# Optimization experiments

Measured on AMD Instinct MI355X. Metric: run time of the kernel, lower is better.

The kernel has to match this reference:

```python
import jax, jax.numpy as jnp
import numpy as np

B, S, D = 2, 2048, 1024
H, HD = 16, 64  # num_heads, hidden_size per head


def setup_inputs() -> dict:
    key = jax.random.key(0)
    ks = jax.random.split(key, 10)
    inp = {
        'queries': jax.random.normal(ks[0], (B, S, D), jnp.float32),
        'keys': jax.random.normal(ks[1], (B, S, D), jnp.float32),
        'values': jax.random.normal(ks[2], (B, S, D), jnp.float32),
        # binary indicator masks (some zeros so renorm guard path is exercised)
        'ind_q': (jax.random.uniform(ks[3], (B, S)) > 0.2).astype(jnp.float32),
        'ind_k': (jax.random.uniform(ks[4], (B, S)) > 0.2).astype(jnp.float32),
        'ind_v': (jax.random.uniform(ks[5], (B, S)) > 0.2).astype(jnp.float32),
        'Wq': jax.random.normal(ks[6], (D, H * HD), jnp.float32) / np.sqrt(D),
        'Wk': jax.random.normal(ks[7], (D, H * HD), jnp.float32) / np.sqrt(D),
        'Wv': jax.random.normal(ks[8], (D, H * HD), jnp.float32) / np.sqrt(D),
        'Wo': jax.random.normal(ks[9], (H * HD, D), jnp.float32) / np.sqrt(H * HD),
    }
    return inp


def reference(queries, keys, values, ind_q, ind_k, ind_v, Wq, Wk, Wv, Wo):
    b, nq, _ = queries.shape
    nk = keys.shape[1]
    # projections -> [B, H, S, HD], masked by indicators
    Q = (queries @ Wq).reshape(b, nq, H, HD).transpose(0, 2, 1, 3) * ind_q[:, None, :, None]
    K = (keys @ Wk).reshape(b, nk, H, HD).transpose(0, 2, 1, 3) * ind_k[:, None, :, None]
    V = (values @ Wv).reshape(b, nk, H, HD).transpose(0, 2, 1, 3) * ind_v[:, None, :, None]
    # scaled dot-product scores, plain softmax over keys
    scores = jnp.einsum('bhqd,bhkd->bhqk', Q, K) / jnp.sqrt(jnp.float32(HD))
    attn = jax.nn.softmax(scores, axis=-1)
    # post-softmax multiplicative key-indicator mask + renormalization with zero-row guard
    attn = attn * ind_k[:, None, None, :]
    denom = jnp.sum(attn, axis=-1, keepdims=True)
    attn = attn / jnp.where(denom == 0.0, 1.0, denom)
    out = jnp.einsum('bhqk,bhkd->bhqd', attn, V)  # [B, H, Q, HD]
    out = out.transpose(0, 2, 1, 3).reshape(b, nq, H * HD)
    return out @ Wo
```

## Files before the change

### kernel.cpp

```cpp
#include <hip/hip_runtime.h>
#include <math.h>

typedef __attribute__((ext_vector_type(8))) short bf16x8;
typedef __attribute__((ext_vector_type(4))) float f32x4;

__device__ __forceinline__ unsigned short f2b(float f) {
    union { float f; unsigned int u; } v; v.f = f;
    unsigned int u = v.u + 0x7FFFu + ((v.u >> 16) & 1u);
    return (unsigned short)(u >> 16);
}

__device__ __forceinline__ unsigned int pack2bf(float a, float b) {
    union { float f; unsigned int u; } ua, ub; ua.f = a; ub.f = b;
    return __builtin_amdgcn_perm(ub.u + 0x8000u, ua.u + 0x8000u, 0x07060302u);
}

__device__ __forceinline__ f32x4 mfma16(bf16x8 a, bf16x8 b, f32x4 c) {
    return __builtin_amdgcn_mfma_f32_16x16x32_bf16(a, b, c, 0, 0, 0);
}

__device__ __forceinline__ void async_ld16(void* l, const void* g) {
    __builtin_amdgcn_global_load_lds(
        (__attribute__((address_space(1))) void*)g,
        (__attribute__((address_space(3))) void*)l, 16, 0, 0);
}

__global__ __launch_bounds__(256) void cvt3(
    const float* __restrict__ q, const float* __restrict__ k,
    const float* __restrict__ v, unsigned short* __restrict__ qo,
    unsigned short* __restrict__ ko, unsigned short* __restrict__ vo)
{
    const int z = blockIdx.z;
    const float* in = (z == 0) ? q : (z == 1) ? k : v;
    unsigned short* out = (z == 0) ? qo : (z == 1) ? ko : vo;
    const int i = (blockIdx.x * 256 + threadIdx.x) * 4;
    const float4 x = *(const float4*)(in + i);
    ushort4 o; o.x = f2b(x.x); o.y = f2b(x.y); o.z = f2b(x.z); o.w = f2b(x.w);
    *(ushort4*)(out + i) = o;
}

__global__ __launch_bounds__(256) void cvt_tr(
    const float* __restrict__ W0, const float* __restrict__ W1,
    const float* __restrict__ W2, const float* __restrict__ W3,
    unsigned short* __restrict__ T0, unsigned short* __restrict__ T1,
    unsigned short* __restrict__ T2, unsigned short* __restrict__ T3)
{
    const int z = blockIdx.z;
    const float* W = (z == 0) ? W0 : (z == 1) ? W1 : (z == 2) ? W2 : W3;
    unsigned short* T = (z == 0) ? T0 : (z == 1) ? T1 : (z == 2) ? T2 : T3;
    __shared__ short Ls[64 * 65];
    const int t = threadIdx.x;
    const int k0 = blockIdx.x * 64, n0 = blockIdx.y * 64;
#pragma unroll
    for (int ii = 0; ii < 4; ++ii) {
        const int kl = (t >> 4) + 16 * ii, nl = (t & 15) * 4;
        const float4 v = *(const float4*)&W[(size_t)(k0 + kl) * 1024 + n0 + nl];
        Ls[kl * 65 + nl + 0] = (short)f2b(v.x);
        Ls[kl * 65 + nl + 1] = (short)f2b(v.y);
        Ls[kl * 65 + nl + 2] = (short)f2b(v.z);
        Ls[kl * 65 + nl + 3] = (short)f2b(v.w);
    }
    __syncthreads();
#pragma unroll
    for (int ii = 0; ii < 4; ++ii) {
        const int nl = (t >> 4) + 16 * ii, kl = (t & 15) * 4;
        ushort4 o;
        o.x = (unsigned short)Ls[(kl + 0) * 65 + nl];
        o.y = (unsigned short)Ls[(kl + 1) * 65 + nl];
        o.z = (unsigned short)Ls[(kl + 2) * 65 + nl];
        o.w = (unsigned short)Ls[(kl + 3) * 65 + nl];
        *(ushort4*)&T[(size_t)(n0 + nl) * 1024 + k0 + kl] = o;
    }
}

__global__ __launch_bounds__(256) void gemm_proj3(
    const unsigned short* __restrict__ qb, const unsigned short* __restrict__ kb,
    const unsigned short* __restrict__ vb,
    const unsigned short* __restrict__ Wqt, const unsigned short* __restrict__ Wkt,
    const unsigned short* __restrict__ Wvt,
    unsigned short* __restrict__ Qw, unsigned short* __restrict__ Kw,
    unsigned short* __restrict__ Vw,
    const float* __restrict__ iq, const float* __restrict__ ik,
    const float* __restrict__ iv)
{
    const int z = blockIdx.z;
    const unsigned short* A  = (z == 0) ? qb  : (z == 1) ? kb  : vb;
    const unsigned short* Bt = (z == 0) ? Wqt : (z == 1) ? Wkt : Wvt;
    unsigned short* Cw       = (z == 0) ? Qw  : (z == 1) ? Kw  : Vw;
    const float* msk         = (z == 0) ? iq  : (z == 1) ? ik  : iv;
    const float scale = (z == 0) ? 0.125f : 1.0f;

    __shared__ __align__(16) short As[128 * 32];
    __shared__ __align__(16) short Bs[128 * 32];
    __shared__ float maskL[128];
    const int t = threadIdx.x;
    const int w = t >> 6, lane = t & 63, l15 = lane & 15, quad = lane >> 4;
    const int wr = w >> 1, wc = w & 1;
    const int n0 = blockIdx.x * 128, m0 = blockIdx.y * 128;
    if (t < 128) maskL[t] = msk[m0 + t] * scale;

    const int srow = lane >> 2, soff = (lane & 3) * 8;

    f32x4 zero4 = {0.f, 0.f, 0.f, 0.f};
    f32x4 acc[4][4];
#pragma unroll
    for (int i = 0; i < 4; ++i)
#pragma unroll
        for (int j = 0; j < 4; ++j) acc[i][j] = zero4;

    for (int k0 = 0; k0 < 1024; k0 += 32) {
        __syncthreads();
#pragma unroll
        for (int i = 0; i < 2; ++i) {
            const int r = 16 * (2 * w + i);
            async_ld16(As + r * 32, A + (size_t)(m0 + r + srow) * 1024 + k0 + soff);
            async_ld16(Bs + r * 32, Bt + (size_t)(n0 + r + srow) * 1024 + k0 + soff);
        }
        __syncthreads();
        bf16x8 af[4], bfr[4];
#pragma unroll
        for (int i = 0; i < 4; ++i)
            af[i] = *(const bf16x8*)&As[(64 * wr + 16 * i + l15) * 32 + 8 * quad];
#pragma unroll
        for (int j = 0; j < 4; ++j)
            bfr[j] = *(const bf16x8*)&Bs[(64 * wc + 16 * j + l15) * 32 + 8 * quad];
#pragma unroll
        for (int i = 0; i < 4; ++i)
#pragma unroll
            for (int j = 0; j < 4; ++j)
                acc[i][j] = mfma16(af[i], bfr[j], acc[i][j]);
    }

    const int h = 2 * blockIdx.x + wc;
#pragma unroll
    for (int i = 0; i < 4; ++i)
#pragma unroll
        for (int j = 0; j < 4; ++j)
#pragma unroll
            for (int reg = 0; reg < 4; ++reg) {
                const int mloc = 64 * wr + 16 * i + 4 * quad + reg;
                const int m = m0 + mloc;
                const int bb = m >> 11, s = m & 2047;
                const int hd = 16 * j + l15;
                Cw[((size_t)(bb * 16 + h) * 2048 + s) * 64 + hd] =
                    f2b(acc[i][j][reg] * maskL[mloc]);
            }
}

__global__ __launch_bounds__(256) void gemm_out(
    const unsigned short* __restrict__ A, const unsigned short* __restrict__ Bt,
    float* __restrict__ C)
{
    __shared__ __align__(16) short As[128 * 32];
    __shared__ __align__(16) short Bs[64 * 32];
    const int t = threadIdx.x;
    const int w = t >> 6, lane = t & 63, l15 = lane & 15, quad = lane >> 4;
    const int wr = w >> 1, wc = w & 1;
    const int n0 = blockIdx.x * 64, m0 = blockIdx.y * 128;
    const int srow = lane >> 2, soff = (lane & 3) * 8;

    f32x4 zero4 = {0.f, 0.f, 0.f, 0.f};
    f32x4 acc[4][2];
#pragma unroll
    for (int i = 0; i < 4; ++i) { acc[i][0] = zero4; acc[i][1] = zero4; }

    for (int k0 = 0; k0 < 1024; k0 += 32) {
        __syncthreads();
#pragma unroll
        for (int i = 0; i < 2; ++i) {
            const int r = 16 * (2 * w + i);
            async_ld16(As + r * 32, A + (size_t)(m0 + r + srow) * 1024 + k0 + soff);
        }
        async_ld16(Bs + (16 * w) * 32, Bt + (size_t)(n0 + 16 * w + srow) * 1024 + k0 + soff);
        __syncthreads();
        bf16x8 af[4], bfr[2];
#pragma unroll
        for (int i = 0; i < 4; ++i)
            af[i] = *(const bf16x8*)&As[(64 * wr + 16 * i + l15) * 32 + 8 * quad];
#pragma unroll
        for (int j = 0; j < 2; ++j)
            bfr[j] = *(const bf16x8*)&Bs[(32 * wc + 16 * j + l15) * 32 + 8 * quad];
#pragma unroll
        for (int i = 0; i < 4; ++i)
#pragma unroll
            for (int j = 0; j < 2; ++j)
                acc[i][j] = mfma16(af[i], bfr[j], acc[i][j]);
    }
#pragma unroll
    for (int i = 0; i < 4; ++i)
#pragma unroll
        for (int j = 0; j < 2; ++j)
#pragma unroll
            for (int reg = 0; reg < 4; ++reg) {
                const int m = m0 + 64 * wr + 16 * i + 4 * quad + reg;
                const int n = n0 + 32 * wc + 16 * j + l15;
                C[(size_t)m * 1024 + n] = acc[i][j][reg];
            }
}

#define GST 72

__global__ __launch_bounds__(512, 4) void attn_mfma(
    const unsigned short* __restrict__ Qw, const unsigned short* __restrict__ Kw,
    const unsigned short* __restrict__ Vw, const float* __restrict__ indk,
    unsigned short* __restrict__ AO)
{
    __shared__ __align__(16) short Ks[2][64 * GST];
    __shared__ __align__(16) short Vt[2][64 * GST];
    __shared__ __align__(16) short Ps[128 * GST];
    __shared__ float biask[2][64];
    const int t = threadIdx.x;
    const int w = t >> 6, lane = t & 63, l15 = lane & 15, quad = lane >> 4;
    const int q0 = blockIdx.x * 128;
    const int h = blockIdx.y, b = blockIdx.z;
    const size_t base = (size_t)(b * 16 + h) * (2048 * 64);
    const unsigned short* Qb = Qw + base + (size_t)q0 * 64;
    const unsigned short* Kb = Kw + base;
    const unsigned short* Vb = Vw + base;

#pragma unroll
    for (int i = 0; i < 4; ++i) {
        const int idx = t + 512 * i;
        const int r = idx >> 4, dg = (idx & 15) * 4;
        *(ushort4*)&Ps[r * GST + dg] = *(const ushort4*)&Qb[r * 64 + dg];
    }
    ushort4 kreg[2], vreg[2];
    float breg = 0.f;
#pragma unroll
    for (int u = 0; u < 2; ++u) {
        const int idx = t + 512 * u;
        kreg[u] = *(const ushort4*)&Kb[(size_t)(idx >> 4) * 64 + (idx & 15) * 4];
        vreg[u] = *(const ushort4*)&Vb[(size_t)(idx & 63) * 64 + (idx >> 6) * 4];
    }
    if (t < 64) breg = indk[b * 2048 + t];
    __syncthreads();
    bf16x8 qf[2];
    qf[0] = *(const bf16x8*)&Ps[(16 * w + l15) * GST + 8 * quad];
    qf[1] = *(const bf16x8*)&Ps[(16 * w + l15) * GST + 32 + 8 * quad];

    f32x4 zero4 = {0.f, 0.f, 0.f, 0.f};
    f32x4 oacc[4];
    oacc[0] = zero4; oacc[1] = zero4; oacc[2] = zero4; oacc[3] = zero4;
    float m_i = -INFINITY, l_i = 0.f;

    for (int c = 0; c < 32; ++c) {
        const int cur = c & 1;
#pragma unroll
        for (int u = 0; u < 2; ++u) {
            const int idx = t + 512 * u;
            const int r = idx >> 4, dg = (idx & 15) * 4;
            *(ushort4*)&Ks[cur][r * GST + dg] = kreg[u];
            const int key = idx & 63, dq = idx >> 6;
            Vt[cur][(4 * dq + 0) * GST + key] = vreg[u].x;
            Vt[cur][(4 * dq + 1) * GST + key] = vreg[u].y;
            Vt[cur][(4 * dq + 2) * GST + key] = vreg[u].z;
            Vt[cur][(4 * dq + 3) * GST + key] = vreg[u].w;
        }
        if (t < 64) biask[cur][t] = (breg != 0.f) ? 0.f : -1e30f;
        __syncthreads();
        {
            const int kn = (c < 31 ? c + 1 : 31) * 64;
#pragma unroll
            for (int u = 0; u < 2; ++u) {
                const int idx = t + 512 * u;
                kreg[u] = *(const ushort4*)&Kb[(size_t)(kn + (idx >> 4)) * 64 + (idx & 15) * 4];
                vreg[u] = *(const ushort4*)&Vb[(size_t)(kn + (idx & 63)) * 64 + (idx >> 6) * 4];
            }
            if (t < 64) breg = indk[b * 2048 + kn + t];
        }
        const short* KsC = Ks[cur];
        const short* VtC = Vt[cur];

        f32x4 sacc[4];
        sacc[0] = zero4; sacc[1] = zero4; sacc[2] = zero4; sacc[3] = zero4;
#pragma unroll
        for (int ks = 0; ks < 2; ++ks)
#pragma unroll
            for (int nj = 0; nj < 4; ++nj) {
                const bf16x8 kf = *(const bf16x8*)&KsC[(16 * nj + l15) * GST + 32 * ks + 8 * quad];
                sacc[nj] = mfma16(kf, qf[ks], sacc[nj]);
            }

#pragma unroll
        for (int nj = 0; nj < 4; ++nj) {
            const float4 bv = *(const float4*)&biask[cur][16 * nj + 4 * quad];
            sacc[nj][0] += bv.x; sacc[nj][1] += bv.y;
            sacc[nj][2] += bv.z; sacc[nj][3] += bv.w;
        }

        float mx = -INFINITY;
#pragma unroll
        for (int nj = 0; nj < 4; ++nj)
#pragma unroll
            for (int r = 0; r < 4; ++r) mx = fmaxf(mx, sacc[nj][r]);
        mx = fmaxf(mx, __shfl_xor(mx, 16));
        mx = fmaxf(mx, __shfl_xor(mx, 32));
        const float mnew = fmaxf(fmaxf(m_i, mx), -1e28f);
        const float alpha = __expf(m_i - mnew);
        float rs = 0.f;
#pragma unroll
        for (int nj = 0; nj < 4; ++nj)
#pragma unroll
            for (int r = 0; r < 4; ++r) {
                const float p = __expf(sacc[nj][r] - mnew);
                sacc[nj][r] = p;
                rs += p;
            }
        rs += __shfl_xor(rs, 16);
        rs += __shfl_xor(rs, 32);
        l_i = l_i * alpha + rs;
        m_i = mnew;

#pragma unroll
        for (int nj = 0; nj < 4; ++nj) {
            uint2 d;
            d.x = pack2bf(sacc[nj][0], sacc[nj][1]);
            d.y = pack2bf(sacc[nj][2], sacc[nj][3]);
            *(uint2*)&Ps[(16 * w + l15) * GST + 16 * nj + 4 * quad] = d;
        }

        float ar[4];
#pragma unroll
        for (int r = 0; r < 4; ++r) ar[r] = __shfl(alpha, 4 * quad + r);
#pragma unroll
        for (int nj = 0; nj < 4; ++nj)
#pragma unroll
            for (int r = 0; r < 4; ++r) oacc[nj][r] *= ar[r];

#pragma unroll
        for (int ks = 0; ks < 2; ++ks) {
            const bf16x8 pa = *(const bf16x8*)&Ps[(16 * w + l15) * GST + 32 * ks + 8 * quad];
#pragma unroll
            for (int nj = 0; nj < 4; ++nj) {
                const bf16x8 vbf = *(const bf16x8*)&VtC[(16 * nj + l15) * GST + 32 * ks + 8 * quad];
                oacc[nj] = mfma16(pa, vbf, oacc[nj]);
            }
        }
    }

    const float inv = (l_i > 0.f) ? 1.f / l_i : 0.f;
    float invr[4];
#pragma unroll
    for (int r = 0; r < 4; ++r) invr[r] = __shfl(inv, 4 * quad + r);
#pragma unroll
    for (int nj = 0; nj < 4; ++nj)
#pragma unroll
        for (int r = 0; r < 4; ++r) {
            const int row = q0 + 16 * w + 4 * quad + r;
            AO[(size_t)(b * 2048 + row) * 1024 + h * 64 + 16 * nj + l15] =
                f2b(oacc[nj][r] * invr[r]);
        }
}

extern "C" void kernel_launch(void* const* d_in, const int* in_sizes, int n_in,
                              void* d_out, int out_size, void* d_ws, size_t ws_size,
                              hipStream_t stream) {
    const float* q  = (const float*)d_in[0];
    const float* k  = (const float*)d_in[1];
    const float* v  = (const float*)d_in[2];
    const float* iq = (const float*)d_in[3];
    const float* ik = (const float*)d_in[4];
    const float* iv = (const float*)d_in[5];
    const float* Wq = (const float*)d_in[6];
    const float* Wk = (const float*)d_in[7];
    const float* Wv = (const float*)d_in[8];
    const float* Wo = (const float*)d_in[9];
    float* out = (float*)d_out;
    unsigned short* ws = (unsigned short*)d_ws;

    const size_t M1 = 1048576;
    unsigned short* qb  = ws;
    unsigned short* kb  = ws + 4  * M1;
    unsigned short* vb  = ws + 8  * M1;
    unsigned short* Wqt = ws + 12 * M1;
    unsigned short* Wkt = ws + 13 * M1;
    unsigned short* Wvt = ws + 14 * M1;
    unsigned short* Wot = ws + 15 * M1;
    unsigned short* Qw  = ws + 16 * M1;
    unsigned short* Kw  = ws + 20 * M1;
    unsigned short* Vw  = ws + 24 * M1;
    unsigned short* AO  = ws + 28 * M1;

    cvt3<<<dim3(4096, 1, 3), dim3(256), 0, stream>>>(q, k, v, qb, kb, vb);
    cvt_tr<<<dim3(16, 16, 4), dim3(256), 0, stream>>>(Wq, Wk, Wv, Wo, Wqt, Wkt, Wvt, Wot);
    gemm_proj3<<<dim3(8, 32, 3), dim3(256), 0, stream>>>(
        qb, kb, vb, Wqt, Wkt, Wvt, Qw, Kw, Vw, iq, ik, iv);
    attn_mfma<<<dim3(16, 16, 2), dim3(512), 0, stream>>>(Qw, Kw, Vw, ik, AO);
    gemm_out<<<dim3(16, 32), dim3(256), 0, stream>>>(AO, Wot, out);
}
```

Before: 256.1 us.

## Keep P in registers, fold log2e into Q, lazy rescale, packed V transpose

Removes the shared-memory round trip for the softmax probabilities. The S accumulator rows are permuted so that each lane's P values can feed the PV MFMA directly as operands. The log2(e) factor is folded into the Q projection scale, so exponentials use the hardware v_exp_f32 and packing uses v_cvt_pk_bf16_f32. The online-softmax rescale of the output accumulator is skipped unless the running max grows by more than 8. The V transpose now writes packed dword stores built with byte permutes, and Q is loaded straight from global into registers. s_setprio hints are placed around the MFMA blocks. This cuts LDS traffic and ALU work, at the cost of bounded growth in the unnormalised exponentials.

```diff
diff --git a/kernel.cpp b/kernel.cpp
--- a/kernel.cpp
+++ b/kernel.cpp
@@ -10,11 +10,6 @@
     return (unsigned short)(u >> 16);
 }
 
-__device__ __forceinline__ unsigned int pack2bf(float a, float b) {
-    union { float f; unsigned int u; } ua, ub; ua.f = a; ub.f = b;
-    return __builtin_amdgcn_perm(ub.u + 0x8000u, ua.u + 0x8000u, 0x07060302u);
-}
-
 __device__ __forceinline__ f32x4 mfma16(bf16x8 a, bf16x8 b, f32x4 c) {
     return __builtin_amdgcn_mfma_f32_16x16x32_bf16(a, b, c, 0, 0, 0);
 }
@@ -23,6 +18,16 @@
     __builtin_amdgcn_global_load_lds(
         (__attribute__((address_space(1))) void*)g,
         (__attribute__((address_space(3))) void*)l, 16, 0, 0);
+}
+
+__device__ __forceinline__ float exp2_hw(float x) {
+    float r; asm("v_exp_f32 %0, %1" : "=v"(r) : "v"(x)); return r;
+}
+
+__device__ __forceinline__ unsigned int cvtpk_bf16(float a, float b) {
+    unsigned int r;
+    asm("v_cvt_pk_bf16_f32 %0, %1, %2" : "=v"(r) : "v"(a), "v"(b));
+    return r;
 }
 
 __global__ __launch_bounds__(256) void cvt3(
@@ -88,7 +93,7 @@
     const unsigned short* Bt = (z == 0) ? Wqt : (z == 1) ? Wkt : Wvt;
     unsigned short* Cw       = (z == 0) ? Qw  : (z == 1) ? Kw  : Vw;
     const float* msk         = (z == 0) ? iq  : (z == 1) ? ik  : iv;
-    const float scale = (z == 0) ? 0.125f : 1.0f;
+    const float scale = (z == 0) ? 0.125f * 1.44269504088896f : 1.0f;
 
     __shared__ __align__(16) short As[128 * 32];
     __shared__ __align__(16) short Bs[128 * 32];
@@ -207,7 +212,6 @@
 {
     __shared__ __align__(16) short Ks[2][64 * GST];
     __shared__ __align__(16) short Vt[2][64 * GST];
-    __shared__ __align__(16) short Ps[128 * GST];
     __shared__ float biask[2][64];
     const int t = threadIdx.x;
     const int w = t >> 6, lane = t & 63, l15 = lane & 15, quad = lane >> 4;
@@ -218,25 +222,24 @@
     const unsigned short* Kb = Kw + base;
     const unsigned short* Vb = Vw + base;
 
-#pragma unroll
-    for (int i = 0; i < 4; ++i) {
-        const int idx = t + 512 * i;
-        const int r = idx >> 4, dg = (idx & 15) * 4;
-        *(ushort4*)&Ps[r * GST + dg] = *(const ushort4*)&Qb[r * 64 + dg];
-    }
+    bf16x8 qf[2];
+    qf[0] = *(const bf16x8*)&Qb[(16 * w + l15) * 64 + 8 * quad];
+    qf[1] = *(const bf16x8*)&Qb[(16 * w + l15) * 64 + 32 + 8 * quad];
+
+    const int dq = t >> 5, kp2 = (t & 31) * 2;
+
     ushort4 kreg[2], vreg[2];
     float breg = 0.f;
 #pragma unroll
     for (int u = 0; u < 2; ++u) {
         const int idx = t + 512 * u;
         kreg[u] = *(const ushort4*)&Kb[(size_t)(idx >> 4) * 64 + (idx & 15) * 4];
-        vreg[u] = *(const ushort4*)&Vb[(size_t)(idx & 63) * 64 + (idx >> 6) * 4];
-    }
+    }
+    vreg[0] = *(const ushort4*)&Vb[(size_t)kp2 * 64 + 4 * dq];
+    vreg[1] = *(const ushort4*)&Vb[(size_t)(kp2 + 1) * 64 + 4 * dq];
     if (t < 64) breg = indk[b * 2048 + t];
-    __syncthreads();
-    bf16x8 qf[2];
-    qf[0] = *(const bf16x8*)&Ps[(16 * w + l15) * GST + 8 * quad];
-    qf[1] = *(const bf16x8*)&Ps[(16 * w + l15) * GST + 32 + 8 * quad];
+
+    const int rbase = 8 * (l15 >> 2) + (l15 & 3);
 
     f32x4 zero4 = {0.f, 0.f, 0.f, 0.f};
     f32x4 oacc[4];
@@ -248,13 +251,19 @@
 #pragma unroll
         for (int u = 0; u < 2; ++u) {
             const int idx = t + 512 * u;
-            const int r = idx >> 4, dg = (idx & 15) * 4;
-            *(ushort4*)&Ks[cur][r * GST + dg] = kreg[u];
-            const int key = idx & 63, dq = idx >> 6;
-            Vt[cur][(4 * dq + 0) * GST + key] = vreg[u].x;
-            Vt[cur][(4 * dq + 1) * GST + key] = vreg[u].y;
-            Vt[cur][(4 * dq + 2) * GST + key] = vreg[u].z;
-            Vt[cur][(4 * dq + 3) * GST + key] = vreg[u].w;
+            *(ushort4*)&Ks[cur][(idx >> 4) * GST + (idx & 15) * 4] = kreg[u];
+        }
+        {
+            const unsigned int* v0d = (const unsigned int*)&vreg[0];
+            const unsigned int* v1d = (const unsigned int*)&vreg[1];
+            *(unsigned int*)&Vt[cur][(4 * dq + 0) * GST + kp2] =
+                __builtin_amdgcn_perm(v1d[0], v0d[0], 0x05040100u);
+            *(unsigned int*)&Vt[cur][(4 * dq + 1) * GST + kp2] =
+                __builtin_amdgcn_perm(v1d[0], v0d[0], 0x07060302u);
+            *(unsigned int*)&Vt[cur][(4 * dq + 2) * GST + kp2] =
+                __builtin_amdgcn_perm(v1d[1], v0d[1], 0x05040100u);
+            *(unsigned int*)&Vt[cur][(4 * dq + 3) * GST + kp2] =
+                __builtin_amdgcn_perm(v1d[1], v0d[1], 0x07060302u);
         }
         if (t < 64) biask[cur][t] = (breg != 0.f) ? 0.f : -1e30f;
         __syncthreads();
@@ -264,78 +273,87 @@
             for (int u = 0; u < 2; ++u) {
                 const int idx = t + 512 * u;
                 kreg[u] = *(const ushort4*)&Kb[(size_t)(kn + (idx >> 4)) * 64 + (idx & 15) * 4];
-                vreg[u] = *(const ushort4*)&Vb[(size_t)(kn + (idx & 63)) * 64 + (idx >> 6) * 4];
             }
+            vreg[0] = *(const ushort4*)&Vb[(size_t)(kn + kp2) * 64 + 4 * dq];
+            vreg[1] = *(const ushort4*)&Vb[(size_t)(kn + kp2 + 1) * 64 + 4 * dq];
             if (t < 64) breg = indk[b * 2048 + kn + t];
         }
         const short* KsC = Ks[cur];
         const short* VtC = Vt[cur];
 
         f32x4 sacc[4];
-        sacc[0] = zero4; sacc[1] = zero4; sacc[2] = zero4; sacc[3] = zero4;
+#pragma unroll
+        for (int g = 0; g < 4; ++g) {
+            const float4 bv = *(const float4*)&biask[cur][32 * (g >> 1) + 4 * (g & 1) + 8 * quad];
+            sacc[g][0] = bv.x; sacc[g][1] = bv.y; sacc[g][2] = bv.z; sacc[g][3] = bv.w;
+        }
+        __builtin_amdgcn_s_setprio(1);
 #pragma unroll
         for (int ks = 0; ks < 2; ++ks)
 #pragma unroll
-            for (int nj = 0; nj < 4; ++nj) {
-                const bf16x8 kf = *(const bf16x8*)&KsC[(16 * nj + l15) * GST + 32 * ks + 8 * quad];
-                sacc[nj] = mfma16(kf, qf[ks], sacc[nj]);
+            for (int g = 0; g < 4; ++g) {
+                const bf16x8 kf = *(const bf16x8*)
+                    &KsC[(32 * (g >> 1) + 4 * (g & 1) + rbase) * GST + 32 * ks + 8 * quad];
+                sacc[g] = mfma16(kf, qf[ks], sacc[g]);
             }
-
-#pragma unroll
-        for (int nj = 0; nj < 4; ++nj) {
-            const float4 bv = *(const float4*)&biask[cur][16 * nj + 4 * quad];
-            sacc[nj][0] += bv.x; sacc[nj][1] += bv.y;
-            sacc[nj][2] += bv.z; sacc[nj][3] += bv.w;
-        }
-
-        float mx = -INFINITY;
-#pragma unroll
-        for (int nj = 0; nj < 4; ++nj)
-#pragma unroll
-            for (int r = 0; r < 4; ++r) mx = fmaxf(mx, sacc[nj][r]);
+        __builtin_amdgcn_s_setprio(0);
+
+        float mg[4];
+#pragma unroll
+        for (int g = 0; g < 4; ++g)
+            mg[g] = fmaxf(fmaxf(sacc[g][0], sacc[g][1]), fmaxf(sacc[g][2], sacc[g][3]));
+        float mx = fmaxf(fmaxf(mg[0], mg[1]), fmaxf(mg[2], mg[3]));
         mx = fmaxf(mx, __shfl_xor(mx, 16));
         mx = fmaxf(mx, __shfl_xor(mx, 32));
-        const float mnew = fmaxf(fmaxf(m_i, mx), -1e28f);
-        const float alpha = __expf(m_i - mnew);
-        float rs = 0.f;
-#pragma unroll
-        for (int nj = 0; nj < 4; ++nj)
-#pragma unroll
-            for (int r = 0; r < 4; ++r) {
-                const float p = __expf(sacc[nj][r] - mnew);
-                sacc[nj][r] = p;
-                rs += p;
+        const float mxc = fmaxf(mx, -1e28f);
+
+        if (!__all(mxc <= m_i + 8.f)) {
+            const float mnew = fmaxf(m_i, mxc);
+            const float alpha = exp2_hw(m_i - mnew);
+            float ar[4];
+#pragma unroll
+            for (int r = 0; r < 4; ++r) ar[r] = __shfl(alpha, 4 * quad + r);
+#pragma unroll
+            for (int g = 0; g < 4; ++g)
+#pragma unroll
+                for (int r = 0; r < 4; ++r) oacc[g][r] *= ar[r];
+            l_i *= alpha;
+            m_i = mnew;
+        }
+
+        unsigned int dw[4][2];
+#pragma unroll
+        for (int g = 0; g < 4; ++g) {
+#pragma unroll
+            for (int r = 0; r < 4; ++r)
+                sacc[g][r] = exp2_hw(sacc[g][r] - m_i);
+            dw[g][0] = cvtpk_bf16(sacc[g][0], sacc[g][1]);
+            dw[g][1] = cvtpk_bf16(sacc[g][2], sacc[g][3]);
+        }
+
+        __builtin_amdgcn_s_setprio(1);
+#pragma unroll
+        for (int ks = 0; ks < 2; ++ks) {
+            union { unsigned int u[4]; bf16x8 b; } pc;
+            pc.u[0] = dw[2 * ks][0];     pc.u[1] = dw[2 * ks][1];
+            pc.u[2] = dw[2 * ks + 1][0]; pc.u[3] = dw[2 * ks + 1][1];
+#pragma unroll
+            for (int nj = 0; nj < 4; ++nj) {
+                const bf16x8 vbf = *(const bf16x8*)
+                    &VtC[(16 * nj + l15) * GST + 32 * ks + 8 * quad];
+                oacc[nj] = mfma16(pc.b, vbf, oacc[nj]);
             }
+        }
+        __builtin_amdgcn_s_setprio(0);
+
+        float rg[4];
+#pragma unroll
+        for (int g = 0; g < 4; ++g)
+            rg[g] = (sacc[g][0] + sacc[g][1]) + (sacc[g][2] + sacc[g][3]);
+        float rs = (rg[0] + rg[1]) + (rg[2] + rg[3]);
         rs += __shfl_xor(rs, 16);
         rs += __shfl_xor(rs, 32);
-        l_i = l_i * alpha + rs;
-        m_i = mnew;
-
-#pragma unroll
-        for (int nj = 0; nj < 4; ++nj) {
-            uint2 d;
-            d.x = pack2bf(sacc[nj][0], sacc[nj][1]);
-            d.y = pack2bf(sacc[nj][2], sacc[nj][3]);
-            *(uint2*)&Ps[(16 * w + l15) * GST + 16 * nj + 4 * quad] = d;
-        }
-
-        float ar[4];
-#pragma unroll
-        for (int r = 0; r < 4; ++r) ar[r] = __shfl(alpha, 4 * quad + r);
-#pragma unroll
-        for (int nj = 0; nj < 4; ++nj)
-#pragma unroll
-            for (int r = 0; r < 4; ++r) oacc[nj][r] *= ar[r];
-
-#pragma unroll
-        for (int ks = 0; ks < 2; ++ks) {
-            const bf16x8 pa = *(const bf16x8*)&Ps[(16 * w + l15) * GST + 32 * ks + 8 * quad];
-#pragma unroll
-            for (int nj = 0; nj < 4; ++nj) {
-                const bf16x8 vbf = *(const bf16x8*)&VtC[(16 * nj + l15) * GST + 32 * ks + 8 * quad];
-                oacc[nj] = mfma16(pa, vbf, oacc[nj]);
-            }
-        }
+        l_i += rs;
     }
 
     const float inv = (l_i > 0.f) ? 1.f / l_i : 0.f;
```

Result: faster. 235.1 us (-8.2%).
